# Performance work log

Measured on AMD Instinct MI355X. Metric: run time of the kernel, lower is better.

## Reference

```python
import jax, jax.numpy as jnp
import numpy as np

B, N, NPOINT, K = 8, 8192, 1024, 32
MLP = [64, 64, 128]
EPS = 1e-5  # torch BatchNorm2d default eps


def setup_inputs() -> dict:
    key = jax.random.key(0)
    ks = jax.random.split(key, 1 + 2 * len(MLP))
    inp = {"xyz": jax.random.normal(ks[0], (B, N, 3), jnp.float32)}
    last = 3
    for i, o in enumerate(MLP):
        inp[f"w{i}"] = jax.random.normal(ks[1 + 2 * i], (o, last), jnp.float32) / np.float32(np.sqrt(last))
        inp[f"b{i}"] = jax.random.normal(ks[2 + 2 * i], (o,), jnp.float32) * 0.01
        inp[f"g{i}"] = jnp.ones((o,), jnp.float32)   # BN weight
        inp[f"be{i}"] = jnp.zeros((o,), jnp.float32)  # BN bias
        last = o
    return inp


def farthest_point_sample(xyz, npoint):
    # Sequential FPS; deterministic start at index 0 (original torch uses randint).
    Bb, Nn, _ = xyz.shape

    def step(carry, _):
        distance, farthest = carry
        centroid = jnp.take_along_axis(xyz, farthest[:, None, None], axis=1)  # [B,1,3]
        dist = jnp.sum((xyz - centroid) ** 2, -1)                              # [B,N]
        distance = jnp.minimum(distance, dist)
        nxt = jnp.argmax(distance, -1)
        return (distance, nxt), farthest

    init = (jnp.full((Bb, Nn), 1e10, xyz.dtype), jnp.zeros((Bb,), jnp.int32))
    _, cents = jax.lax.scan(step, init, None, length=npoint)
    return cents.T  # [B, npoint]


def _forward(xyz, params):
    fps_idx = farthest_point_sample(xyz, NPOINT)
    fps_idx = jax.lax.stop_gradient(fps_idx)
    new_xyz = jnp.take_along_axis(xyz, fps_idx[:, :, None], axis=1)  # [B,npoint,3]
    # squared pairwise distances [B, npoint, N]
    d = (jnp.sum(new_xyz ** 2, -1)[:, :, None]
         + jnp.sum(xyz ** 2, -1)[:, None, :]
         - 2.0 * jnp.einsum('bmc,bnc->bmn', new_xyz, xyz))
    _, idx = jax.lax.top_k(-d, K)  # k nearest neighbors, [B,npoint,k]
    grouped = jax.vmap(lambda pts, i: pts[i])(xyz, idx)  # [B,npoint,k,3]
    feat = grouped - new_xyz[:, :, None, :]              # grouped_xyz_norm
    # 1x1 Conv2d + BatchNorm2d(training stats) + ReLU stack
    for (w, b, g, be) in params:
        feat = jnp.einsum('bnkc,oc->bnko', feat, w) + b
        mu = jnp.mean(feat, axis=(0, 1, 2))
        var = jnp.var(feat, axis=(0, 1, 2))
        feat = g * (feat - mu) * jax.lax.rsqrt(var + EPS) + be
        feat = jax.nn.relu(feat)
    out = jnp.max(feat, axis=2)             # max over k neighbors -> [B,npoint,Cout]
    return new_xyz, jnp.transpose(out, (0, 2, 1))  # [B,npoint,3], [B,Cout,npoint]


def reference(xyz, w0, b0, g0, be0, w1, b1, g1, be1, w2, b2, g2, be2):
    params = [(w0, b0, g0, be0), (w1, b1, g1, be1), (w2, b2, g2, be2)]
    return _forward(xyz, params)
```

## Files before the change

kernel.cpp:

```cpp
#include <hip/hip_runtime.h>

#define NN_ 8192
#define MM_ 1024

#define DPP_UMAX64(K, CTRL)                                                     \
  {                                                                             \
    const int lo_ = (int)(unsigned int)(K);                                     \
    const int hi_ = (int)(unsigned int)((K) >> 32);                             \
    const int slo_ = __builtin_amdgcn_update_dpp(lo_, lo_, (CTRL), 0xf, 0xf, false); \
    const int shi_ = __builtin_amdgcn_update_dpp(hi_, hi_, (CTRL), 0xf, 0xf, false); \
    const unsigned long long ok_ =                                              \
        ((unsigned long long)(unsigned int)shi_ << 32) | (unsigned int)slo_;    \
    (K) = (ok_ > (K)) ? ok_ : (K);                                              \
  }
#define DPP_UMIN64(K, CTRL)                                                     \
  {                                                                             \
    const int lo_ = (int)(unsigned int)(K);                                     \
    const int hi_ = (int)(unsigned int)((K) >> 32);                             \
    const int slo_ = __builtin_amdgcn_update_dpp(lo_, lo_, (CTRL), 0xf, 0xf, false); \
    const int shi_ = __builtin_amdgcn_update_dpp(hi_, hi_, (CTRL), 0xf, 0xf, false); \
    const unsigned long long ok_ =                                              \
        ((unsigned long long)(unsigned int)shi_ << 32) | (unsigned int)slo_;    \
    (K) = (ok_ < (K)) ? ok_ : (K);                                              \
  }

#define WAVE_STATS(T, ACC, PO_S, PO_Q)                                          \
  {                                                                             \
    _Pragma("unroll") for (int o_ = 0; o_ < 64; ++o_)                           \
        (T)[o_ * 64 + ((lane + o_) & 63)] = (ACC)[o_];                          \
    float s_ = 0.0f, q_ = 0.0f;                                                 \
    _Pragma("unroll") for (int j_ = 0; j_ < 64; ++j_) {                         \
      const float v_ = (T)[lane * 64 + ((j_ + lane) & 63)];                     \
      s_ += v_;                                                                 \
      q_ = fmaf(v_, v_, q_);                                                    \
    }                                                                           \
    (PO_S)[lane] = s_;                                                          \
    (PO_Q)[lane] = q_;                                                          \
  }

__global__ __launch_bounds__(256, 1) void fps_kernel(const float* __restrict__ xyz,
                                                     float* __restrict__ dout) {
  const int b = blockIdx.x;
  const int tid = threadIdx.x;
  const float* xb = xyz + (size_t)b * NN_ * 3;

  __shared__ float s_x[NN_], s_y[NN_], s_z[NN_];
  __shared__ float s_out[3 * MM_];
  __shared__ __align__(16) unsigned long long s_key[2][4];

  for (int i = tid; i < NN_; i += 256) {
    s_x[i] = xb[3 * i + 0];
    s_y[i] = xb[3 * i + 1];
    s_z[i] = xb[3 * i + 2];
  }
  __syncthreads();

  const int base = 32 * tid;
  float4 rx[8], ry[8], rz[8];
#pragma unroll
  for (int q = 0; q < 8; ++q) {
    rx[q] = *(const float4*)&s_x[base + 4 * q];
    ry[q] = *(const float4*)&s_y[base + 4 * q];
    rz[q] = *(const float4*)&s_z[base + 4 * q];
  }
  asm volatile("" ::: "memory");

  float pd[32];
#pragma unroll
  for (int j = 0; j < 32; ++j) pd[j] = 1e10f;

  const int lane = tid & 63;
  const int wv = tid >> 6;

  float cx = s_x[0], cy = s_y[0], cz = s_z[0];

  for (int it = 0; it < MM_; ++it) {
    if (tid == 0) {
      s_out[it * 3 + 0] = cx;
      s_out[it * 3 + 1] = cy;
      s_out[it * 3 + 2] = cz;
    }
    if (it == MM_ - 1) break;

    float ld = -1.0f;
    int lj = 0;
#define FPS_UPD(PX, PY, PZ, J)                                                 \
    {                                                                          \
      const float dx = __fsub_rn(PX, cx);                                      \
      const float dy = __fsub_rn(PY, cy);                                      \
      const float dz = __fsub_rn(PZ, cz);                                      \
      const float dist = __fadd_rn(                                            \
          __fadd_rn(__fmul_rn(dx, dx), __fmul_rn(dy, dy)), __fmul_rn(dz, dz)); \
      const float nd = fminf(pd[J], dist);                                     \
      pd[J] = nd;                                                              \
      if (nd > ld) { ld = nd; lj = (J); }                                      \
    }
#pragma unroll
    for (int q = 0; q < 8; ++q) {
      FPS_UPD(rx[q].x, ry[q].x, rz[q].x, 4 * q + 0)
      FPS_UPD(rx[q].y, ry[q].y, rz[q].y, 4 * q + 1)
      FPS_UPD(rx[q].z, ry[q].z, rz[q].z, 4 * q + 2)
      FPS_UPD(rx[q].w, ry[q].w, rz[q].w, 4 * q + 3)
    }
#undef FPS_UPD

    unsigned long long key =
        ((unsigned long long)__float_as_uint(ld) << 32) |
        (unsigned int)(8191 - (base + lj));
    DPP_UMAX64(key, 0x111)
    DPP_UMAX64(key, 0x112)
    DPP_UMAX64(key, 0x114)
    DPP_UMAX64(key, 0x118)
    DPP_UMAX64(key, 0x142)
    DPP_UMAX64(key, 0x143)
    if (lane == 63) s_key[it & 1][wv] = key;
    __syncthreads();

    const ulonglong2 ka = *(const ulonglong2*)&s_key[it & 1][0];
    const ulonglong2 kb = *(const ulonglong2*)&s_key[it & 1][2];
    unsigned long long best = (ka.x > ka.y) ? ka.x : ka.y;
    const unsigned long long bb = (kb.x > kb.y) ? kb.x : kb.y;
    best = (best > bb) ? best : bb;
    const int win = 8191 - (int)(unsigned int)(best & 0xFFFFFFFFu);
    cx = s_x[win];
    cy = s_y[win];
    cz = s_z[win];
  }

  __syncthreads();
  float* outx = dout + (size_t)b * MM_ * 3;
#pragma unroll
  for (int i = 0; i < 12; ++i) outx[i * 256 + tid] = s_out[i * 256 + tid];
}

__global__ __launch_bounds__(64) void knn_kernel(const float* __restrict__ xyz,
                                                 const float* __restrict__ dout,
                                                 int* __restrict__ knn) {
  __shared__ float dl[128][64];
  const int lane = threadIdx.x;
  const int center = blockIdx.x;
  const int b = center >> 10;
  const int m = center & 1023;
  const float* xb = xyz + (size_t)b * NN_ * 3;
  const float* cp = dout + (size_t)b * MM_ * 3 + m * 3;
  const float cx = cp[0], cy = cp[1], cz = cp[2];
  const float sm = __fadd_rn(__fadd_rn(__fmul_rn(cx, cx), __fmul_rn(cy, cy)),
                             __fmul_rn(cz, cz));

  float gd[16];
  int gj[16];
#pragma unroll
  for (int g = 0; g < 16; ++g) {
#pragma unroll
    for (int t = 0; t < 8; ++t) {
      const int jj = g * 8 + t;
      const int p = jj * 64 + lane;
      const float x = xb[p * 3 + 0];
      const float y = xb[p * 3 + 1];
      const float z = xb[p * 3 + 2];
      const float sn = __fadd_rn(__fadd_rn(__fmul_rn(x, x), __fmul_rn(y, y)),
                                 __fmul_rn(z, z));
      const float dt = __fmaf_rn(cz, z, __fmaf_rn(cy, y, __fmul_rn(cx, x)));
      const float d = __fsub_rn(__fadd_rn(sm, sn), __fmul_rn(2.0f, dt));
      dl[jj][lane] = d;
      if (t == 0) { gd[g] = d; gj[g] = jj; }
      else if (d < gd[g]) { gd[g] = d; gj[g] = jj; }
    }
  }

  int out_p = 0;
  const float INF = __int_as_float(0x7f800000);
  for (int r = 0; r < 32; ++r) {
    float ldv = gd[0];
    int ljj = gj[0];
#pragma unroll
    for (int g = 1; g < 16; ++g) {
      if (gd[g] < ldv) { ldv = gd[g]; ljj = gj[g]; }
    }
    const int lp0 = ljj * 64 + lane;
    const unsigned db = __float_as_uint(ldv);
    const unsigned mono = (db & 0x80000000u) ? ~db : (db | 0x80000000u);
    unsigned long long kk =
        ((unsigned long long)mono << 32) | (unsigned int)lp0;
    DPP_UMIN64(kk, 0x111)
    DPP_UMIN64(kk, 0x112)
    DPP_UMIN64(kk, 0x114)
    DPP_UMIN64(kk, 0x118)
    DPP_UMIN64(kk, 0x142)
    DPP_UMIN64(kk, 0x143)
    const int lp = __builtin_amdgcn_readlane((int)(unsigned int)(kk & 0xFFFFFFFFull), 63);
    if (lane == r) out_p = lp;
    const int wl = lp & 63;
    if (lane == wl) {
      const int jjs = lp >> 6;
      const int gs = jjs >> 3;
      dl[jjs][lane] = INF;
      float md = INF;
      int mj = 0;
#pragma unroll
      for (int t = 0; t < 8; ++t) {
        const int jj2 = gs * 8 + t;
        const float v = dl[jj2][lane];
        if (v < md) { md = v; mj = jj2; }
      }
#pragma unroll
      for (int g = 0; g < 16; ++g) {
        if (g == gs) { gd[g] = md; gj[g] = mj; }
      }
    }
  }
  if (lane < 32) knn[center * 32 + lane] = out_p;
}

__global__ void prep_kernel(const float* __restrict__ w1, const float* __restrict__ w2,
                            float* __restrict__ w1t, float* __restrict__ w2t) {
  const int t = blockIdx.x * 256 + threadIdx.x;
  if (t < 4096) { const int o = t >> 6, c = t & 63; w1t[c * 64 + o] = w1[t]; }
  if (t < 8192) { const int o = t >> 6, c = t & 63; w2t[c * 128 + o] = w2[t]; }
}

__global__ __launch_bounds__(256) void s1_kernel(const float* __restrict__ xyz,
                                                 const float* __restrict__ dout,
                                                 const int* __restrict__ knn,
                                                 const float* __restrict__ w0,
                                                 const float* __restrict__ b0,
                                                 float* __restrict__ part1) {
  __shared__ float tw[4 * 4096];
  const int tid = threadIdx.x;
  const int r = blockIdx.x * 256 + tid;
  const int cid = r >> 5;
  const int b = cid >> 10;
  const int m = cid & 1023;
  const int idx = knn[r];
  const float* pp = xyz + ((size_t)b * NN_ + idx) * 3;
  const float* cc = dout + ((size_t)b * MM_ + m) * 3;
  const float fx = pp[0] - cc[0];
  const float fy = pp[1] - cc[1];
  const float fz = pp[2] - cc[2];
  float acc[64];
#pragma unroll
  for (int o = 0; o < 64; ++o)
    acc[o] = fmaf(w0[o * 3 + 2], fz, fmaf(w0[o * 3 + 1], fy, fmaf(w0[o * 3 + 0], fx, b0[o])));
  const int lane = tid & 63;
  const int wv = tid >> 6;
  float* T = &tw[wv * 4096];
  float* po = part1 + ((size_t)blockIdx.x * 4 + wv) * 128;
  WAVE_STATS(T, acc, po, po + 64)
}

__global__ __launch_bounds__(256) void rstat_kernel(const float* __restrict__ part, int C,
                                                    const float* __restrict__ g,
                                                    const float* __restrict__ be,
                                                    float* __restrict__ sc,
                                                    float* __restrict__ sh) {
  const int c = blockIdx.x;
  const int tid = threadIdx.x;
  float S = 0.0f, Q = 0.0f;
  for (int i = tid; i < 4096; i += 256) {
    S += part[(size_t)i * 2 * C + c];
    Q += part[(size_t)i * 2 * C + C + c];
  }
  const int lane = tid & 63;
#pragma unroll
  for (int mk = 1; mk < 64; mk <<= 1) { S += __shfl_xor(S, mk, 64); Q += __shfl_xor(Q, mk, 64); }
  __shared__ float rs[4], rq[4];
  if (lane == 0) { rs[tid >> 6] = S; rq[tid >> 6] = Q; }
  __syncthreads();
  if (tid == 0) {
    S = rs[0] + rs[1] + rs[2] + rs[3];
    Q = rq[0] + rq[1] + rq[2] + rq[3];
    const float mean = S * (1.0f / 262144.0f);
    const float var = fmaf(-mean, mean, Q * (1.0f / 262144.0f));
    const float s = g[c] * rsqrtf(var + 1e-5f);
    sc[c] = s;
    sh[c] = fmaf(-mean, s, be[c]);
  }
}

template <int STAGE>
__global__ __launch_bounds__(256) void chain_kernel(
    const float* __restrict__ xyz, const float* __restrict__ dout,
    const int* __restrict__ knn,
    const float* __restrict__ w0, const float* __restrict__ b0,
    const float* __restrict__ w1t, const float* __restrict__ b1,
    const float* __restrict__ w2t, const float* __restrict__ b2,
    const float* __restrict__ sc1, const float* __restrict__ sh1,
    const float* __restrict__ sc2, const float* __restrict__ sh2,
    const float* __restrict__ sc3, const float* __restrict__ sh3,
    float* __restrict__ part, float* __restrict__ outp) {
  __shared__ float f[64 * 256];
  const int tid = threadIdx.x;
  const int r = blockIdx.x * 256 + tid;
  const int cid = r >> 5;
  const int b = cid >> 10;
  const int m = cid & 1023;
  const int idx = knn[r];
  const float* pp = xyz + ((size_t)b * NN_ + idx) * 3;
  const float* cc = dout + ((size_t)b * MM_ + m) * 3;
  const float fx = pp[0] - cc[0];
  const float fy = pp[1] - cc[1];
  const float fz = pp[2] - cc[2];
  const int lane = tid & 63;
  const int wv = tid >> 6;
  float acc[64];
#pragma unroll
  for (int o = 0; o < 64; ++o)
    acc[o] = fmaf(w0[o * 3 + 2], fz, fmaf(w0[o * 3 + 1], fy, fmaf(w0[o * 3 + 0], fx, b0[o])));
#pragma unroll
  for (int o = 0; o < 64; ++o)
    f[o * 256 + tid] = fmaxf(fmaf(acc[o], sc1[o], sh1[o]), 0.0f);
  float a2[64];
#pragma unroll
  for (int o = 0; o < 64; ++o) a2[o] = b1[o];
#pragma unroll 4
  for (int c = 0; c < 64; ++c) {
    const float x = f[c * 256 + tid];
#pragma unroll
    for (int o = 0; o < 64; ++o) a2[o] = fmaf(w1t[c * 64 + o], x, a2[o]);
  }
  if constexpr (STAGE == 2) {
    __syncthreads();
    float* T = &f[wv * 4096];
    float* po = part + ((size_t)blockIdx.x * 4 + wv) * 128;
    WAVE_STATS(T, a2, po, po + 64)
    return;
  }
#pragma unroll
  for (int o = 0; o < 64; ++o)
    f[o * 256 + tid] = fmaxf(fmaf(a2[o], sc2[o], sh2[o]), 0.0f);
  if constexpr (STAGE == 3) {
    float a3l[64], a3h[64];
#pragma unroll
    for (int o = 0; o < 64; ++o) { a3l[o] = b2[o]; a3h[o] = b2[64 + o]; }
#pragma unroll 2
    for (int c = 0; c < 64; ++c) {
      const float x = f[c * 256 + tid];
#pragma unroll
      for (int o = 0; o < 64; ++o) a3l[o] = fmaf(w2t[c * 128 + o], x, a3l[o]);
#pragma unroll
      for (int o = 0; o < 64; ++o) a3h[o] = fmaf(w2t[c * 128 + 64 + o], x, a3h[o]);
    }
    __syncthreads();
    float* T = &f[wv * 4096];
    float* po = part + ((size_t)blockIdx.x * 4 + wv) * 256;
    WAVE_STATS(T, a3l, po, po + 128)
    WAVE_STATS(T, a3h, po + 64, po + 192)
    return;
  }
#pragma unroll
  for (int h = 0; h < 2; ++h) {
    float a3[64];
#pragma unroll
    for (int o = 0; o < 64; ++o) a3[o] = b2[h * 64 + o];
#pragma unroll 4
    for (int c = 0; c < 64; ++c) {
      const float x = f[c * 256 + tid];
#pragma unroll
      for (int o = 0; o < 64; ++o) a3[o] = fmaf(w2t[c * 128 + h * 64 + o], x, a3[o]);
    }
#pragma unroll
    for (int o = 0; o < 64; ++o) {
      float v = fmaxf(fmaf(a3[o], sc3[h * 64 + o], sh3[h * 64 + o]), 0.0f);
#pragma unroll
      for (int mk = 1; mk < 32; mk <<= 1) v = fmaxf(v, __shfl_xor(v, mk, 64));
      if ((lane & 31) == 0)
        outp[24576 + (size_t)b * 131072 + (size_t)(h * 64 + o) * 1024 + m] = v;
    }
  }
}

extern "C" void kernel_launch(void* const* d_in, const int* in_sizes, int n_in,
                              void* d_out, int out_size, void* d_ws, size_t ws_size,
                              hipStream_t stream) {
  const float* xyz = (const float*)d_in[0];
  const float* w0 = (const float*)d_in[1];
  const float* b0 = (const float*)d_in[2];
  const float* g0 = (const float*)d_in[3];
  const float* be0 = (const float*)d_in[4];
  const float* w1 = (const float*)d_in[5];
  const float* b1 = (const float*)d_in[6];
  const float* g1 = (const float*)d_in[7];
  const float* be1 = (const float*)d_in[8];
  const float* w2 = (const float*)d_in[9];
  const float* b2 = (const float*)d_in[10];
  const float* g2 = (const float*)d_in[11];
  const float* be2 = (const float*)d_in[12];
  float* out = (float*)d_out;
  char* ws = (char*)d_ws;

  int* knn = (int*)ws;
  float* part1 = (float*)(ws + (size_t)1 * (1 << 20));
  float* part2 = (float*)(ws + (size_t)3 * (1 << 20));
  float* part3 = (float*)(ws + (size_t)5 * (1 << 20));
  float* sc1 = (float*)(ws + (size_t)9 * (1 << 20));
  float* sh1 = sc1 + 64;
  float* sc2 = sh1 + 64;
  float* sh2 = sc2 + 64;
  float* sc3 = sh2 + 64;
  float* sh3 = sc3 + 128;
  float* w1t = sh3 + 128;
  float* w2t = w1t + 4096;

  fps_kernel<<<8, 256, 0, stream>>>(xyz, out);
  knn_kernel<<<8192, 64, 0, stream>>>(xyz, out, knn);
  prep_kernel<<<32, 256, 0, stream>>>(w1, w2, w1t, w2t);
  s1_kernel<<<1024, 256, 0, stream>>>(xyz, out, knn, w0, b0, part1);
  rstat_kernel<<<64, 256, 0, stream>>>(part1, 64, g0, be0, sc1, sh1);
  chain_kernel<2><<<1024, 256, 0, stream>>>(xyz, out, knn, w0, b0, w1t, b1, w2t, b2,
                                            sc1, sh1, sc2, sh2, sc3, sh3, part2, out);
  rstat_kernel<<<64, 256, 0, stream>>>(part2, 64, g1, be1, sc2, sh2);
  chain_kernel<3><<<1024, 256, 0, stream>>>(xyz, out, knn, w0, b0, w1t, b1, w2t, b2,
                                            sc1, sh1, sc2, sh2, sc3, sh3, part3, out);
  rstat_kernel<<<128, 256, 0, stream>>>(part3, 128, g2, be2, sc3, sh3);
  chain_kernel<4><<<1024, 256, 0, stream>>>(xyz, out, knn, w0, b0, w1t, b1, w2t, b2,
                                            sc1, sh1, sc2, sh2, sc3, sh3, part3, out);
}
```

Before: 1.506 ms.

## Cache layer-2 pre-BN activations in workspace and split FPS argmax into max then index search

```diff
diff --git a/kernel.cpp b/kernel.cpp
--- a/kernel.cpp
+++ b/kernel.cpp
@@ -2,6 +2,7 @@
 
 #define NN_ 8192
 #define MM_ 1024
+#define NROWS_ 262144
 
 #define DPP_UMAX64(K, CTRL)                                                     \
   {                                                                             \
@@ -82,9 +83,8 @@
     }
     if (it == MM_ - 1) break;
 
-    float ld = -1.0f;
-    int lj = 0;
-#define FPS_UPD(PX, PY, PZ, J)                                                 \
+    float mx0 = -1.0f, mx1 = -1.0f, mx2 = -1.0f, mx3 = -1.0f;
+#define FPS_UPD(PX, PY, PZ, J, MACC)                                           \
     {                                                                          \
       const float dx = __fsub_rn(PX, cx);                                      \
       const float dy = __fsub_rn(PY, cy);                                      \
@@ -93,20 +93,38 @@
           __fadd_rn(__fmul_rn(dx, dx), __fmul_rn(dy, dy)), __fmul_rn(dz, dz)); \
       const float nd = fminf(pd[J], dist);                                     \
       pd[J] = nd;                                                              \
-      if (nd > ld) { ld = nd; lj = (J); }                                      \
+      MACC = fmaxf(MACC, nd);                                                  \
     }
 #pragma unroll
     for (int q = 0; q < 8; ++q) {
-      FPS_UPD(rx[q].x, ry[q].x, rz[q].x, 4 * q + 0)
-      FPS_UPD(rx[q].y, ry[q].y, rz[q].y, 4 * q + 1)
-      FPS_UPD(rx[q].z, ry[q].z, rz[q].z, 4 * q + 2)
-      FPS_UPD(rx[q].w, ry[q].w, rz[q].w, 4 * q + 3)
+      FPS_UPD(rx[q].x, ry[q].x, rz[q].x, 4 * q + 0, mx0)
+      FPS_UPD(rx[q].y, ry[q].y, rz[q].y, 4 * q + 1, mx1)
+      FPS_UPD(rx[q].z, ry[q].z, rz[q].z, 4 * q + 2, mx2)
+      FPS_UPD(rx[q].w, ry[q].w, rz[q].w, 4 * q + 3, mx3)
     }
 #undef FPS_UPD
+    const float m = fmaxf(fmaxf(mx0, mx1), fmaxf(mx2, mx3));
+
+    unsigned u16[16];
+#pragma unroll
+    for (int i = 0; i < 16; ++i) {
+      const unsigned a = (pd[i] == m) ? (unsigned)i : 1023u;
+      const unsigned c = (pd[i + 16] == m) ? (unsigned)(i + 16) : 1023u;
+      u16[i] = (a < c) ? a : c;
+    }
+    unsigned u8[8];
+#pragma unroll
+    for (int i = 0; i < 8; ++i) u8[i] = (u16[i] < u16[i + 8]) ? u16[i] : u16[i + 8];
+    unsigned u4[4];
+#pragma unroll
+    for (int i = 0; i < 4; ++i) u4[i] = (u8[i] < u8[i + 4]) ? u8[i] : u8[i + 4];
+    const unsigned u2a = (u4[0] < u4[2]) ? u4[0] : u4[2];
+    const unsigned u2b = (u4[1] < u4[3]) ? u4[1] : u4[3];
+    const unsigned lj = (u2a < u2b) ? u2a : u2b;
 
     unsigned long long key =
-        ((unsigned long long)__float_as_uint(ld) << 32) |
-        (unsigned int)(8191 - (base + lj));
+        ((unsigned long long)__float_as_uint(m) << 32) |
+        (unsigned int)(8191 - (base + (int)lj));
     DPP_UMAX64(key, 0x111)
     DPP_UMAX64(key, 0x112)
     DPP_UMAX64(key, 0x114)
@@ -287,38 +305,50 @@
     const float* __restrict__ sc1, const float* __restrict__ sh1,
     const float* __restrict__ sc2, const float* __restrict__ sh2,
     const float* __restrict__ sc3, const float* __restrict__ sh3,
-    float* __restrict__ part, float* __restrict__ outp) {
+    float* __restrict__ part, float* __restrict__ outp,
+    float* __restrict__ a2g, int cached) {
   __shared__ float f[64 * 256];
   const int tid = threadIdx.x;
   const int r = blockIdx.x * 256 + tid;
   const int cid = r >> 5;
   const int b = cid >> 10;
   const int m = cid & 1023;
-  const int idx = knn[r];
-  const float* pp = xyz + ((size_t)b * NN_ + idx) * 3;
-  const float* cc = dout + ((size_t)b * MM_ + m) * 3;
-  const float fx = pp[0] - cc[0];
-  const float fy = pp[1] - cc[1];
-  const float fz = pp[2] - cc[2];
   const int lane = tid & 63;
   const int wv = tid >> 6;
-  float acc[64];
-#pragma unroll
-  for (int o = 0; o < 64; ++o)
-    acc[o] = fmaf(w0[o * 3 + 2], fz, fmaf(w0[o * 3 + 1], fy, fmaf(w0[o * 3 + 0], fx, b0[o])));
-#pragma unroll
-  for (int o = 0; o < 64; ++o)
-    f[o * 256 + tid] = fmaxf(fmaf(acc[o], sc1[o], sh1[o]), 0.0f);
+
   float a2[64];
-#pragma unroll
-  for (int o = 0; o < 64; ++o) a2[o] = b1[o];
+  if (STAGE == 2 || !cached) {
+    const int idx = knn[r];
+    const float* pp = xyz + ((size_t)b * NN_ + idx) * 3;
+    const float* cc = dout + ((size_t)b * MM_ + m) * 3;
+    const float fx = pp[0] - cc[0];
+    const float fy = pp[1] - cc[1];
+    const float fz = pp[2] - cc[2];
+    float acc[64];
+#pragma unroll
+    for (int o = 0; o < 64; ++o)
+      acc[o] = fmaf(w0[o * 3 + 2], fz, fmaf(w0[o * 3 + 1], fy, fmaf(w0[o * 3 + 0], fx, b0[o])));
+#pragma unroll
+    for (int o = 0; o < 64; ++o)
+      f[o * 256 + tid] = fmaxf(fmaf(acc[o], sc1[o], sh1[o]), 0.0f);
+#pragma unroll
+    for (int o = 0; o < 64; ++o) a2[o] = b1[o];
 #pragma unroll 4
-  for (int c = 0; c < 64; ++c) {
-    const float x = f[c * 256 + tid];
-#pragma unroll
-    for (int o = 0; o < 64; ++o) a2[o] = fmaf(w1t[c * 64 + o], x, a2[o]);
-  }
+    for (int c = 0; c < 64; ++c) {
+      const float x = f[c * 256 + tid];
+#pragma unroll
+      for (int o = 0; o < 64; ++o) a2[o] = fmaf(w1t[c * 64 + o], x, a2[o]);
+    }
+  } else {
+#pragma unroll
+    for (int o = 0; o < 64; ++o) a2[o] = a2g[(size_t)o * NROWS_ + r];
+  }
+
   if constexpr (STAGE == 2) {
+    if (cached) {
+#pragma unroll
+      for (int o = 0; o < 64; ++o) a2g[(size_t)o * NROWS_ + r] = a2[o];
+    }
     __syncthreads();
     float* T = &f[wv * 4096];
     float* po = part + ((size_t)blockIdx.x * 4 + wv) * 128;
@@ -400,6 +430,8 @@
   float* sh3 = sc3 + 128;
   float* w1t = sh3 + 128;
   float* w2t = w1t + 4096;
+  float* a2g = (float*)(ws + ((size_t)16 << 20));
+  const int cached = (ws_size >= ((size_t)81 << 20)) ? 1 : 0;
 
   fps_kernel<<<8, 256, 0, stream>>>(xyz, out);
   knn_kernel<<<8192, 64, 0, stream>>>(xyz, out, knn);
@@ -407,11 +439,14 @@
   s1_kernel<<<1024, 256, 0, stream>>>(xyz, out, knn, w0, b0, part1);
   rstat_kernel<<<64, 256, 0, stream>>>(part1, 64, g0, be0, sc1, sh1);
   chain_kernel<2><<<1024, 256, 0, stream>>>(xyz, out, knn, w0, b0, w1t, b1, w2t, b2,
-                                            sc1, sh1, sc2, sh2, sc3, sh3, part2, out);
+                                            sc1, sh1, sc2, sh2, sc3, sh3, part2, out,
+                                            a2g, cached);
   rstat_kernel<<<64, 256, 0, stream>>>(part2, 64, g1, be1, sc2, sh2);
   chain_kernel<3><<<1024, 256, 0, stream>>>(xyz, out, knn, w0, b0, w1t, b1, w2t, b2,
-                                            sc1, sh1, sc2, sh2, sc3, sh3, part3, out);
+                                            sc1, sh1, sc2, sh2, sc3, sh3, part3, out,
+                                            a2g, cached);
   rstat_kernel<<<128, 256, 0, stream>>>(part3, 128, g2, be2, sc3, sh3);
   chain_kernel<4><<<1024, 256, 0, stream>>>(xyz, out, knn, w0, b0, w1t, b1, w2t, b2,
-                                            sc1, sh1, sc2, sh2, sc3, sh3, part3, out);
-}
+                                            sc1, sh1, sc2, sh2, sc3, sh3, part3, out,
+                                            a2g, cached);
+}
```

Result: slower. 1.585 ms (+5.2%).

## Cache layer-2 pre-BN activations in workspace and incrementalize kNN key update

Applied to the files above, without the earlier changes.

```diff
diff --git a/kernel.cpp b/kernel.cpp
--- a/kernel.cpp
+++ b/kernel.cpp
@@ -2,6 +2,7 @@
 
 #define NN_ 8192
 #define MM_ 1024
+#define NROWS_ 262144
 
 #define DPP_UMAX64(K, CTRL)                                                     \
   {                                                                             \
@@ -168,20 +169,21 @@
     }
   }
 
+  float ldv = gd[0];
+  int ljj = gj[0];
+#pragma unroll
+  for (int g = 1; g < 16; ++g) {
+    if (gd[g] < ldv) { ldv = gd[g]; ljj = gj[g]; }
+  }
+  unsigned db = __float_as_uint(ldv);
+  unsigned mono = (db & 0x80000000u) ? ~db : (db | 0x80000000u);
+  unsigned long long mykey =
+      ((unsigned long long)mono << 32) | (unsigned int)(ljj * 64 + lane);
+
   int out_p = 0;
   const float INF = __int_as_float(0x7f800000);
   for (int r = 0; r < 32; ++r) {
-    float ldv = gd[0];
-    int ljj = gj[0];
-#pragma unroll
-    for (int g = 1; g < 16; ++g) {
-      if (gd[g] < ldv) { ldv = gd[g]; ljj = gj[g]; }
-    }
-    const int lp0 = ljj * 64 + lane;
-    const unsigned db = __float_as_uint(ldv);
-    const unsigned mono = (db & 0x80000000u) ? ~db : (db | 0x80000000u);
-    unsigned long long kk =
-        ((unsigned long long)mono << 32) | (unsigned int)lp0;
+    unsigned long long kk = mykey;
     DPP_UMIN64(kk, 0x111)
     DPP_UMIN64(kk, 0x112)
     DPP_UMIN64(kk, 0x114)
@@ -207,6 +209,16 @@
       for (int g = 0; g < 16; ++g) {
         if (g == gs) { gd[g] = md; gj[g] = mj; }
       }
+      float nldv = gd[0];
+      int nljj = gj[0];
+#pragma unroll
+      for (int g = 1; g < 16; ++g) {
+        if (gd[g] < nldv) { nldv = gd[g]; nljj = gj[g]; }
+      }
+      const unsigned ndb = __float_as_uint(nldv);
+      const unsigned nmono = (ndb & 0x80000000u) ? ~ndb : (ndb | 0x80000000u);
+      mykey = ((unsigned long long)nmono << 32) |
+              (unsigned int)(nljj * 64 + lane);
     }
   }
   if (lane < 32) knn[center * 32 + lane] = out_p;
@@ -287,38 +299,50 @@
     const float* __restrict__ sc1, const float* __restrict__ sh1,
     const float* __restrict__ sc2, const float* __restrict__ sh2,
     const float* __restrict__ sc3, const float* __restrict__ sh3,
-    float* __restrict__ part, float* __restrict__ outp) {
+    float* __restrict__ part, float* __restrict__ outp,
+    float* __restrict__ a2g, int cached) {
   __shared__ float f[64 * 256];
   const int tid = threadIdx.x;
   const int r = blockIdx.x * 256 + tid;
   const int cid = r >> 5;
   const int b = cid >> 10;
   const int m = cid & 1023;
-  const int idx = knn[r];
-  const float* pp = xyz + ((size_t)b * NN_ + idx) * 3;
-  const float* cc = dout + ((size_t)b * MM_ + m) * 3;
-  const float fx = pp[0] - cc[0];
-  const float fy = pp[1] - cc[1];
-  const float fz = pp[2] - cc[2];
   const int lane = tid & 63;
   const int wv = tid >> 6;
-  float acc[64];
-#pragma unroll
-  for (int o = 0; o < 64; ++o)
-    acc[o] = fmaf(w0[o * 3 + 2], fz, fmaf(w0[o * 3 + 1], fy, fmaf(w0[o * 3 + 0], fx, b0[o])));
-#pragma unroll
-  for (int o = 0; o < 64; ++o)
-    f[o * 256 + tid] = fmaxf(fmaf(acc[o], sc1[o], sh1[o]), 0.0f);
+
   float a2[64];
-#pragma unroll
-  for (int o = 0; o < 64; ++o) a2[o] = b1[o];
+  if (STAGE == 2 || !cached) {
+    const int idx = knn[r];
+    const float* pp = xyz + ((size_t)b * NN_ + idx) * 3;
+    const float* cc = dout + ((size_t)b * MM_ + m) * 3;
+    const float fx = pp[0] - cc[0];
+    const float fy = pp[1] - cc[1];
+    const float fz = pp[2] - cc[2];
+    float acc[64];
+#pragma unroll
+    for (int o = 0; o < 64; ++o)
+      acc[o] = fmaf(w0[o * 3 + 2], fz, fmaf(w0[o * 3 + 1], fy, fmaf(w0[o * 3 + 0], fx, b0[o])));
+#pragma unroll
+    for (int o = 0; o < 64; ++o)
+      f[o * 256 + tid] = fmaxf(fmaf(acc[o], sc1[o], sh1[o]), 0.0f);
+#pragma unroll
+    for (int o = 0; o < 64; ++o) a2[o] = b1[o];
 #pragma unroll 4
-  for (int c = 0; c < 64; ++c) {
-    const float x = f[c * 256 + tid];
-#pragma unroll
-    for (int o = 0; o < 64; ++o) a2[o] = fmaf(w1t[c * 64 + o], x, a2[o]);
-  }
+    for (int c = 0; c < 64; ++c) {
+      const float x = f[c * 256 + tid];
+#pragma unroll
+      for (int o = 0; o < 64; ++o) a2[o] = fmaf(w1t[c * 64 + o], x, a2[o]);
+    }
+  } else {
+#pragma unroll
+    for (int o = 0; o < 64; ++o) a2[o] = a2g[(size_t)o * NROWS_ + r];
+  }
+
   if constexpr (STAGE == 2) {
+    if (cached) {
+#pragma unroll
+      for (int o = 0; o < 64; ++o) a2g[(size_t)o * NROWS_ + r] = a2[o];
+    }
     __syncthreads();
     float* T = &f[wv * 4096];
     float* po = part + ((size_t)blockIdx.x * 4 + wv) * 128;
@@ -400,6 +424,8 @@
   float* sh3 = sc3 + 128;
   float* w1t = sh3 + 128;
   float* w2t = w1t + 4096;
+  float* a2g = (float*)(ws + ((size_t)16 << 20));
+  const int cached = (ws_size >= ((size_t)81 << 20)) ? 1 : 0;
 
   fps_kernel<<<8, 256, 0, stream>>>(xyz, out);
   knn_kernel<<<8192, 64, 0, stream>>>(xyz, out, knn);
@@ -407,11 +433,14 @@
   s1_kernel<<<1024, 256, 0, stream>>>(xyz, out, knn, w0, b0, part1);
   rstat_kernel<<<64, 256, 0, stream>>>(part1, 64, g0, be0, sc1, sh1);
   chain_kernel<2><<<1024, 256, 0, stream>>>(xyz, out, knn, w0, b0, w1t, b1, w2t, b2,
-                                            sc1, sh1, sc2, sh2, sc3, sh3, part2, out);
+                                            sc1, sh1, sc2, sh2, sc3, sh3, part2, out,
+                                            a2g, cached);
   rstat_kernel<<<64, 256, 0, stream>>>(part2, 64, g1, be1, sc2, sh2);
   chain_kernel<3><<<1024, 256, 0, stream>>>(xyz, out, knn, w0, b0, w1t, b1, w2t, b2,
-                                            sc1, sh1, sc2, sh2, sc3, sh3, part3, out);
+                                            sc1, sh1, sc2, sh2, sc3, sh3, part3, out,
+                                            a2g, cached);
   rstat_kernel<<<128, 256, 0, stream>>>(part3, 128, g2, be2, sc3, sh3);
   chain_kernel<4><<<1024, 256, 0, stream>>>(xyz, out, knn, w0, b0, w1t, b1, w2t, b2,
-                                            sc1, sh1, sc2, sh2, sc3, sh3, part3, out);
-}
+                                            sc1, sh1, sc2, sh2, sc3, sh3, part3, out,
+                                            a2g, cached);
+}
```

Result: no change. 1.481 ms (median of 2 runs) (-1.6%).
